# Kernel tuning notes

Measured on AMD Instinct MI355X. Metric: run time of the kernel, lower is better.

Reference implementation:

```python
import jax, jax.numpy as jnp
import numpy as np

B, C, H, W_ = 4, 3, 224, 224
K = 196          # max_segments
E = 768          # embed_dim


def setup_inputs() -> dict:
    key = jax.random.key(0)
    k1, k2, k3 = jax.random.split(key, 3)
    img = jax.random.normal(k1, (B, C, H, W_), dtype=jnp.float32)
    segments = jax.random.randint(k2, (B, H, W_), 0, K, dtype=jnp.int32)
    W = jax.random.normal(k3, (C, E), dtype=jnp.float32) * 0.02
    b = jnp.zeros((E,), dtype=jnp.float32)
    return {"img": img, "segments": segments, "W": W, "b": b}


def reference(img, segments, W, b):
    # Per-segment one-hot masked bucketing (the torch loop, vectorized):
    # segment_features[b,k,c,h,w] = img[b,c,h,w] * (segments[b,h,w] == k)
    onehot = jax.nn.one_hot(segments, K, dtype=img.dtype)           # (B,H,W,K)
    seg_feat = jnp.einsum('bhwk,bchw->bkchw', onehot, img)          # (B,K,C,H,W)
    # Feature extractor stand-in: spatial mean pool + linear C->E
    pooled = seg_feat.mean(axis=(3, 4))                              # (B,K,C)
    out = jnp.einsum('bkc,ce->bke', pooled, W) + b                   # (B,K,E)
    return out
```

## Files before the change

### kernel.cpp

```cpp
#include <hip/hip_runtime.h>

#define Bn  4
#define Cn  3
#define Hn  224
#define Wn  224
#define Kn  196
#define En  768
#define HW  (Hn * Wn)
#define BPB 49
#define NPOOL (Bn * BPB)
#define KC  (Kn * Cn)

__global__ __launch_bounds__(256) void seg_pool_partial(
    const float* __restrict__ img,
    const int*   __restrict__ seg,
    float*       __restrict__ partials)
{
    __shared__ float acc[KC];
    const int tid = threadIdx.x;
    for (int i = tid; i < KC; i += 256) acc[i] = 0.0f;
    __syncthreads();

    const int batch = blockIdx.x / BPB;
    const int blk   = blockIdx.x % BPB;
    const int p4    = blk * 256 + tid;

    const int4*   seg4 = (const int4*)(seg + (size_t)batch * HW);
    const float4* im   = (const float4*)(img + (size_t)batch * Cn * HW);

    const int4   s  = seg4[p4];
    const float4 v0 = im[p4];
    const float4 v1 = im[HW / 4 + p4];
    const float4 v2 = im[2 * (HW / 4) + p4];

    atomicAdd(&acc[s.x * 3 + 0], v0.x);
    atomicAdd(&acc[s.x * 3 + 1], v1.x);
    atomicAdd(&acc[s.x * 3 + 2], v2.x);
    atomicAdd(&acc[s.y * 3 + 0], v0.y);
    atomicAdd(&acc[s.y * 3 + 1], v1.y);
    atomicAdd(&acc[s.y * 3 + 2], v2.y);
    atomicAdd(&acc[s.z * 3 + 0], v0.z);
    atomicAdd(&acc[s.z * 3 + 1], v1.z);
    atomicAdd(&acc[s.z * 3 + 2], v2.z);
    atomicAdd(&acc[s.w * 3 + 0], v0.w);
    atomicAdd(&acc[s.w * 3 + 1], v1.w);
    atomicAdd(&acc[s.w * 3 + 2], v2.w);
    __syncthreads();

    float4* dst = (float4*)(partials + (size_t)blockIdx.x * KC);
    if (tid < KC / 4) dst[tid] = ((const float4*)acc)[tid];
}

__global__ __launch_bounds__(192) void embed_kernel(
    const float* __restrict__ partials,
    const float* __restrict__ Wm,
    const float* __restrict__ bias,
    float*       __restrict__ out)
{
    __shared__ float part[BPB * 3];
    __shared__ float sums[3];
    const int b   = blockIdx.x / Kn;
    const int k   = blockIdx.x % Kn;
    const int tid = threadIdx.x;

    if (tid < BPB * 3) {
        const int j = tid / 3;
        const int c = tid % 3;
        part[tid] = partials[(size_t)(b * BPB + j) * KC + k * 3 + c];
    }
    __syncthreads();

    if (tid < 3) {
        float s = 0.0f;
        #pragma unroll
        for (int j = 0; j < BPB; ++j) s += part[j * 3 + tid];
        sums[tid] = s * (1.0f / (float)HW);
    }
    __syncthreads();

    const float p0 = sums[0];
    const float p1 = sums[1];
    const float p2 = sums[2];

    const float4 w0 = ((const float4*)(Wm          ))[tid];
    const float4 w1 = ((const float4*)(Wm +     En ))[tid];
    const float4 w2 = ((const float4*)(Wm + 2 * En ))[tid];
    const float4 bb = ((const float4*)bias)[tid];

    float4 r;
    r.x = p0 * w0.x + p1 * w1.x + p2 * w2.x + bb.x;
    r.y = p0 * w0.y + p1 * w1.y + p2 * w2.y + bb.y;
    r.z = p0 * w0.z + p1 * w1.z + p2 * w2.z + bb.z;
    r.w = p0 * w0.w + p1 * w1.w + p2 * w2.w + bb.w;
    ((float4*)out)[(size_t)blockIdx.x * (En / 4) + tid] = r;
}

extern "C" void kernel_launch(void* const* d_in, const int* in_sizes, int n_in,
                              void* d_out, int out_size, void* d_ws, size_t ws_size,
                              hipStream_t stream) {
    const float* img  = (const float*)d_in[0];
    const int*   seg  = (const int*)  d_in[1];
    const float* Wm   = (const float*)d_in[2];
    const float* bias = (const float*)d_in[3];
    float* out      = (float*)d_out;
    float* partials = (float*)d_ws;

    seg_pool_partial<<<NPOOL, 256, 0, stream>>>(img, seg, partials);
    embed_kernel<<<Bn * Kn, 192, 0, stream>>>(partials, Wm, bias, out);
}
```

Baseline: 66.37 us.

## Fuse pooling and embedding into one cooperative kernel with grid sync

New measurement: 214.1 us. 3.23x slower.

```diff
diff --git a/kernel.cpp b/kernel.cpp
--- a/kernel.cpp
+++ b/kernel.cpp
@@ -1,4 +1,7 @@
 #include <hip/hip_runtime.h>
+#include <hip/hip_cooperative_groups.h>
+
+namespace cg = cooperative_groups;
 
 #define Bn  4
 #define Cn  3
@@ -10,89 +13,93 @@
 #define BPB 49
 #define NPOOL (Bn * BPB)
 #define KC  (Kn * Cn)
+#define NBLK (Bn * Kn)
 
-__global__ __launch_bounds__(256) void seg_pool_partial(
+__global__ __launch_bounds__(256) void fused_kernel(
     const float* __restrict__ img,
     const int*   __restrict__ seg,
+    const float* __restrict__ Wm,
+    const float* __restrict__ bias,
+    float*       __restrict__ out,
     float*       __restrict__ partials)
 {
-    __shared__ float acc[KC];
+    __shared__ float sh[KC];
+    __shared__ float sums[3];
     const int tid = threadIdx.x;
-    for (int i = tid; i < KC; i += 256) acc[i] = 0.0f;
+
+    if (blockIdx.x < NPOOL) {
+        for (int i = tid; i < KC; i += 256) sh[i] = 0.0f;
+        __syncthreads();
+
+        const int batch = blockIdx.x / BPB;
+        const int blk   = blockIdx.x % BPB;
+        const int p4    = blk * 256 + tid;
+
+        const int4*   seg4 = (const int4*)(seg + (size_t)batch * HW);
+        const float4* im   = (const float4*)(img + (size_t)batch * Cn * HW);
+
+        const int4   s  = seg4[p4];
+        const float4 v0 = im[p4];
+        const float4 v1 = im[HW / 4 + p4];
+        const float4 v2 = im[2 * (HW / 4) + p4];
+
+        atomicAdd(&sh[s.x * 3 + 0], v0.x);
+        atomicAdd(&sh[s.x * 3 + 1], v1.x);
+        atomicAdd(&sh[s.x * 3 + 2], v2.x);
+        atomicAdd(&sh[s.y * 3 + 0], v0.y);
+        atomicAdd(&sh[s.y * 3 + 1], v1.y);
+        atomicAdd(&sh[s.y * 3 + 2], v2.y);
+        atomicAdd(&sh[s.z * 3 + 0], v0.z);
+        atomicAdd(&sh[s.z * 3 + 1], v1.z);
+        atomicAdd(&sh[s.z * 3 + 2], v2.z);
+        atomicAdd(&sh[s.w * 3 + 0], v0.w);
+        atomicAdd(&sh[s.w * 3 + 1], v1.w);
+        atomicAdd(&sh[s.w * 3 + 2], v2.w);
+        __syncthreads();
+
+        float4* dst = (float4*)(partials + (size_t)blockIdx.x * KC);
+        if (tid < KC / 4) dst[tid] = ((const float4*)sh)[tid];
+    }
+
+    __threadfence();
+    cg::this_grid().sync();
     __syncthreads();
 
-    const int batch = blockIdx.x / BPB;
-    const int blk   = blockIdx.x % BPB;
-    const int p4    = blk * 256 + tid;
-
-    const int4*   seg4 = (const int4*)(seg + (size_t)batch * HW);
-    const float4* im   = (const float4*)(img + (size_t)batch * Cn * HW);
-
-    const int4   s  = seg4[p4];
-    const float4 v0 = im[p4];
-    const float4 v1 = im[HW / 4 + p4];
-    const float4 v2 = im[2 * (HW / 4) + p4];
-
-    atomicAdd(&acc[s.x * 3 + 0], v0.x);
-    atomicAdd(&acc[s.x * 3 + 1], v1.x);
-    atomicAdd(&acc[s.x * 3 + 2], v2.x);
-    atomicAdd(&acc[s.y * 3 + 0], v0.y);
-    atomicAdd(&acc[s.y * 3 + 1], v1.y);
-    atomicAdd(&acc[s.y * 3 + 2], v2.y);
-    atomicAdd(&acc[s.z * 3 + 0], v0.z);
-    atomicAdd(&acc[s.z * 3 + 1], v1.z);
-    atomicAdd(&acc[s.z * 3 + 2], v2.z);
-    atomicAdd(&acc[s.w * 3 + 0], v0.w);
-    atomicAdd(&acc[s.w * 3 + 1], v1.w);
-    atomicAdd(&acc[s.w * 3 + 2], v2.w);
-    __syncthreads();
-
-    float4* dst = (float4*)(partials + (size_t)blockIdx.x * KC);
-    if (tid < KC / 4) dst[tid] = ((const float4*)acc)[tid];
-}
-
-__global__ __launch_bounds__(192) void embed_kernel(
-    const float* __restrict__ partials,
-    const float* __restrict__ Wm,
-    const float* __restrict__ bias,
-    float*       __restrict__ out)
-{
-    __shared__ float part[BPB * 3];
-    __shared__ float sums[3];
-    const int b   = blockIdx.x / Kn;
-    const int k   = blockIdx.x % Kn;
-    const int tid = threadIdx.x;
+    const int b = blockIdx.x / Kn;
+    const int k = blockIdx.x % Kn;
 
     if (tid < BPB * 3) {
         const int j = tid / 3;
         const int c = tid % 3;
-        part[tid] = partials[(size_t)(b * BPB + j) * KC + k * 3 + c];
+        sh[tid] = partials[(size_t)(b * BPB + j) * KC + k * 3 + c];
     }
     __syncthreads();
 
     if (tid < 3) {
         float s = 0.0f;
         #pragma unroll
-        for (int j = 0; j < BPB; ++j) s += part[j * 3 + tid];
+        for (int j = 0; j < BPB; ++j) s += sh[j * 3 + tid];
         sums[tid] = s * (1.0f / (float)HW);
     }
     __syncthreads();
 
-    const float p0 = sums[0];
-    const float p1 = sums[1];
-    const float p2 = sums[2];
+    if (tid < En / 4) {
+        const float p0 = sums[0];
+        const float p1 = sums[1];
+        const float p2 = sums[2];
 
-    const float4 w0 = ((const float4*)(Wm          ))[tid];
-    const float4 w1 = ((const float4*)(Wm +     En ))[tid];
-    const float4 w2 = ((const float4*)(Wm + 2 * En ))[tid];
-    const float4 bb = ((const float4*)bias)[tid];
+        const float4 w0 = ((const float4*)(Wm          ))[tid];
+        const float4 w1 = ((const float4*)(Wm +     En ))[tid];
+        const float4 w2 = ((const float4*)(Wm + 2 * En ))[tid];
+        const float4 bb = ((const float4*)bias)[tid];
 
-    float4 r;
-    r.x = p0 * w0.x + p1 * w1.x + p2 * w2.x + bb.x;
-    r.y = p0 * w0.y + p1 * w1.y + p2 * w2.y + bb.y;
-    r.z = p0 * w0.z + p1 * w1.z + p2 * w2.z + bb.z;
-    r.w = p0 * w0.w + p1 * w1.w + p2 * w2.w + bb.w;
-    ((float4*)out)[(size_t)blockIdx.x * (En / 4) + tid] = r;
+        float4 r;
+        r.x = p0 * w0.x + p1 * w1.x + p2 * w2.x + bb.x;
+        r.y = p0 * w0.y + p1 * w1.y + p2 * w2.y + bb.y;
+        r.z = p0 * w0.z + p1 * w1.z + p2 * w2.z + bb.z;
+        r.w = p0 * w0.w + p1 * w1.w + p2 * w2.w + bb.w;
+        ((float4*)out)[(size_t)blockIdx.x * (En / 4) + tid] = r;
+    }
 }
 
 extern "C" void kernel_launch(void* const* d_in, const int* in_sizes, int n_in,
@@ -105,6 +112,8 @@
     float* out      = (float*)d_out;
     float* partials = (float*)d_ws;
 
-    seg_pool_partial<<<NPOOL, 256, 0, stream>>>(img, seg, partials);
-    embed_kernel<<<Bn * Kn, 192, 0, stream>>>(partials, Wm, bias, out);
+    void* args[] = {(void*)&img, (void*)&seg, (void*)&Wm, (void*)&bias,
+                    (void*)&out, (void*)&partials};
+    (void)hipLaunchCooperativeKernel((const void*)fused_kernel, dim3(NBLK),
+                                     dim3(256), args, 0, stream);
 }
```
